# Optimization experiments

Measured on AMD Instinct MI355X. Metric: run time of the kernel, lower is better.

Reference implementation:

```python
import jax, jax.numpy as jnp
import numpy as np

B, S, D = 2, 2048, 2048
H, HD = 16, 128
ROPE_THETA = 10000.0


def _rope_cos_sin(seq_len, head_dim, dtype=jnp.float32):
    inv_freq = 1.0 / (ROPE_THETA ** (jnp.arange(0, head_dim, 2, dtype=jnp.float32) / head_dim))
    t = jnp.arange(seq_len, dtype=jnp.float32)
    freqs = jnp.outer(t, inv_freq)                     # [S, HD/2]
    emb = jnp.concatenate([freqs, freqs], axis=-1)     # [S, HD]
    return jnp.cos(emb).astype(dtype), jnp.sin(emb).astype(dtype)


def _rotate_half(x):
    x1, x2 = jnp.split(x, 2, axis=-1)
    return jnp.concatenate([-x2, x1], axis=-1)


def _apply_rope(x, cos, sin):
    # x: [B, S, H, HD]; cos/sin: [S, HD] -> broadcast over batch and heads
    c = cos[None, :, None, :]
    s = sin[None, :, None, :]
    return x * c + _rotate_half(x) * s


def setup_inputs() -> dict:
    key = jax.random.key(0)
    ks = jax.random.split(key, 6)
    scale = 1.0 / np.sqrt(D)
    hidden_states = jax.random.normal(ks[0], (B, S, D), dtype=jnp.float32)
    # causal additive mask: 0 on/below diagonal, large negative above
    neg = jnp.finfo(jnp.float32).min
    causal = jnp.where(jnp.tril(jnp.ones((S, S), dtype=bool)), 0.0, neg)
    attention_mask = jnp.broadcast_to(causal[None, None, :, :], (B, 1, S, S)).astype(jnp.float32)
    Wq = jax.random.normal(ks[1], (D, D), dtype=jnp.float32) * scale
    Wk = jax.random.normal(ks[2], (D, D), dtype=jnp.float32) * scale
    Wv = jax.random.normal(ks[3], (D, D), dtype=jnp.float32) * scale
    Wo = jax.random.normal(ks[4], (D, D), dtype=jnp.float32) * scale
    return {"hidden_states": hidden_states, "attention_mask": attention_mask,
            "Wq": Wq, "Wk": Wk, "Wv": Wv, "Wo": Wo}


def reference(hidden_states, attention_mask, Wq, Wk, Wv, Wo):
    b, s, d = hidden_states.shape
    # projections (torch Linear: x @ W^T)
    q = (hidden_states @ Wq.T).reshape(b, s, H, HD)
    k = (hidden_states @ Wk.T).reshape(b, s, H, HD)
    v = (hidden_states @ Wv.T).reshape(b, s, H, HD)
    cos, sin = _rope_cos_sin(s, HD, hidden_states.dtype)
    q = _apply_rope(q, cos, sin)
    k = _apply_rope(k, cos, sin)
    # naive attention, [B, H, S, S] scores materialized as in the original
    scores = jnp.einsum('bqhd,bkhd->bhqk', q, k) / np.sqrt(HD)
    scores = scores + attention_mask
    attn = jax.nn.softmax(scores, axis=-1)
    out = jnp.einsum('bhqk,bkhd->bqhd', attn, v).reshape(b, s, d)
    return out @ Wo.T
```

## Files before the change

### kernel.cpp

```cpp
#include <hip/hip_runtime.h>
#include <hip/hip_bf16.h>

typedef __hip_bfloat16 bf16;
typedef __attribute__((ext_vector_type(8))) short s16x8;
typedef __attribute__((ext_vector_type(4))) float f32x4;
typedef __attribute__((ext_vector_type(16))) float f32x16;

#define MFMA16(a, b, c) __builtin_amdgcn_mfma_f32_16x16x32_bf16(a, b, c, 0, 0, 0)
#define MFMA32(a, b, c) __builtin_amdgcn_mfma_f32_32x32x16_bf16(a, b, c, 0, 0, 0)

#define GLL16(gsrc, ldst)                                                                 \
  __builtin_amdgcn_global_load_lds(                                                       \
      (const __attribute__((address_space(1))) unsigned int*)(gsrc),                      \
      (__attribute__((address_space(3))) unsigned int*)(ldst), 16, 0, 0)

#define VMCNT(n) asm volatile("s_waitcnt vmcnt(" #n ")" ::: "memory")
#define BARRIER() __builtin_amdgcn_s_barrier()

static constexpr int S_LEN = 2048;
static constexpr int D_DIM = 2048;
static constexpr int NY = 6144;

union BF4 { ushort4 u; bf16 b[4]; };

__device__ inline unsigned pack2(float a, float b) {
  union { bf16 h[2]; unsigned u; } x;
  x.h[0] = __float2bfloat16(a);
  x.h[1] = __float2bfloat16(b);
  return x.u;
}

__global__ void convert_all(const float* __restrict__ X, const float* __restrict__ Wq,
                            const float* __restrict__ Wk, const float* __restrict__ Wv,
                            const float* __restrict__ Wo, bf16* __restrict__ Xb,
                            bf16* __restrict__ Wb, bf16* __restrict__ Wob,
                            float* __restrict__ cosT, float* __restrict__ sinT) {
  int gid = blockIdx.x * 256 + threadIdx.x;
  if (gid < 6291456) {
    int i4 = gid * 4;
    const float* src;
    bf16* dst;
    int off;
    if (i4 < 8388608) {
      src = X; dst = Xb; off = i4;
    } else {
      int j = i4 - 8388608;
      int seg = j >> 22;
      off = j & 4194303;
      if (seg == 0) { src = Wq; dst = Wb; }
      else if (seg == 1) { src = Wk; dst = Wb + 4194304; }
      else if (seg == 2) { src = Wv; dst = Wb + 8388608; }
      else { src = Wo; dst = Wob; }
    }
    float4 v = *(const float4*)(src + off);
    BF4 o;
    o.b[0] = __float2bfloat16(v.x);
    o.b[1] = __float2bfloat16(v.y);
    o.b[2] = __float2bfloat16(v.z);
    o.b[3] = __float2bfloat16(v.w);
    *(ushort4*)(dst + off) = o.u;
  } else {
    int t4 = (gid - 6291456) * 4;
    if (t4 < 131072) {
#pragma unroll
      for (int k = 0; k < 4; ++k) {
        int i = t4 + k;
        int d = i & 63, s = i >> 6;
        float inv = powf(10000.0f, -(float)d * (1.0f / 64.0f));
        float ang = (float)s * inv;
        cosT[i] = cosf(ang);
        sinT[i] = sinf(ang);
      }
    }
  }
}

__global__ __launch_bounds__(256) void rope_tv(bf16* __restrict__ Y,
                                               const float* __restrict__ cosT,
                                               const float* __restrict__ sinT,
                                               bf16* __restrict__ Vt) {
  __shared__ bf16 tile[32][36];
  const int bid = blockIdx.x;
  const int t = threadIdx.x;
  if (bid < 8192) {
    int idx = bid * 256 + t;
    int quad = idx & 15;
    int h = (idx >> 4) & 15;
    int m = (idx >> 8) & 4095;
    int g = idx >> 20;
    int s = m & (S_LEN - 1);
    int d0 = quad * 4;
    float sc = g ? 1.0f : 0.08838834764831845f;
    bf16* p = Y + (size_t)m * NY + g * D_DIM + h * 128 + d0;
    BF4 lo, hi, olo, ohi;
    lo.u = *(const ushort4*)p;
    hi.u = *(const ushort4*)(p + 64);
    float4 c = *(const float4*)(cosT + s * 64 + d0);
    float4 sn = *(const float4*)(sinT + s * 64 + d0);
    float cc[4] = {c.x, c.y, c.z, c.w};
    float ss[4] = {sn.x, sn.y, sn.z, sn.w};
#pragma unroll
    for (int i = 0; i < 4; ++i) {
      float x1 = __bfloat162float(lo.b[i]);
      float x2 = __bfloat162float(hi.b[i]);
      olo.b[i] = __float2bfloat16((x1 * cc[i] - x2 * ss[i]) * sc);
      ohi.b[i] = __float2bfloat16((x2 * cc[i] + x1 * ss[i]) * sc);
    }
    *(ushort4*)p = olo.u;
    *(ushort4*)(p + 64) = ohi.u;
  } else {
    int id = bid - 8192;
    int bx = id & 63, by = (id >> 6) & 3, bh = id >> 8;
    int b = bh >> 4, h = bh & 15;
    int s0 = bx * 32, d0 = by * 32;
    int r = t >> 3;
    int c4 = (t & 7) * 4;
    BF4 in;
    in.u = *(const ushort4*)(Y + (size_t)(b * S_LEN + s0 + r) * NY + 4096 + h * 128 + d0 + c4);
    *(ushort4*)(&tile[r][c4]) = in.u;
    __syncthreads();
    BF4 o;
#pragma unroll
    for (int i = 0; i < 4; ++i) o.b[i] = tile[c4 + i][r];
    *(ushort4*)(Vt + (size_t)bh * 128 * S_LEN + (size_t)(d0 + r) * S_LEN + s0 + c4) = o.u;
  }
}

__device__ inline void storeC(float* p, float v) { *p = v; }
__device__ inline void storeC(bf16* p, float v) { *p = __float2bfloat16(v); }

template <typename OutT>
__global__ __launch_bounds__(512, 2) void gemm_fine(const bf16* __restrict__ A,
                                                    const bf16* __restrict__ Bm,
                                                    OutT* __restrict__ C, int K, int lda,
                                                    int ldb, int ldc, int mt) {
  __shared__ __align__(16) char lds[147456];
  char* b0 = lds;
  char* b1 = lds + 49152;
  char* b2 = lds + 98304;
  const int tid = threadIdx.x;
  const int lane = tid & 63;
  const int w = tid >> 6;
  const int wm = w >> 2, wn = w & 3;
  const int l15 = lane & 15, lh4 = lane >> 4;
  const int xr = l15 & 7;
  const int xo0 = ((lh4 ^ xr) << 4);
  const int xo1 = (((4 + lh4) ^ xr) << 4);

  const int nwg = gridDim.x;
  const int bid = blockIdx.x;
  const int swz = (bid & 7) * (nwg >> 3) + (bid >> 3);
  const int bm = swz % mt, bn = swz / mt;
  const int row0 = bm * 128, col0 = bn * 256;

  const int srow = w * 8 + (lane >> 3);
  const int scol = ((lane & 7) ^ (lane >> 3)) * 8;
  const bf16* gA = A + (size_t)(row0 + srow) * lda + scol;
  const bf16* gB = Bm + (size_t)(col0 + srow) * ldb + scol;
  const int ldst = w * 1024;

  f32x4 acc[4][4];
#pragma unroll
  for (int i = 0; i < 4; ++i)
#pragma unroll
    for (int j = 0; j < 4; ++j) acc[i][j] = (f32x4){0.f, 0.f, 0.f, 0.f};

  s16x8 af[4], bfr[4];

#define PH_READ(BUF, XO)                                                          \
  _Pragma("unroll") for (int ii = 0; ii < 4; ++ii)                                \
      af[ii] = *(const s16x8*)((BUF) + (wm * 64 + ii * 16 + l15) * 128 + (XO));   \
  _Pragma("unroll") for (int jj = 0; jj < 4; ++jj)                                \
      bfr[jj] = *(const s16x8*)((BUF) + 16384 + (wn * 64 + jj * 16 + l15) * 128 + (XO));
#define PH_FMA()                                                                  \
  __builtin_amdgcn_s_setprio(1);                                                  \
  _Pragma("unroll") for (int jj = 0; jj < 4; ++jj)                                \
  _Pragma("unroll") for (int ii = 0; ii < 4; ++ii)                                \
      acc[ii][jj] = MFMA16(af[ii], bfr[jj], acc[ii][jj]);                         \
  __builtin_amdgcn_s_setprio(0);
#define STAGE_T(BUF, kS)                                                          \
  GLL16(gA + (kS), (BUF) + ldst);                                                 \
  GLL16(gA + (size_t)64 * lda + (kS), (BUF) + 8192 + ldst);                       \
  GLL16(gB + (kS), (BUF) + 16384 + ldst);                                         \
  GLL16(gB + (size_t)64 * ldb + (kS), (BUF) + 24576 + ldst);                      \
  GLL16(gB + (size_t)128 * ldb + (kS), (BUF) + 32768 + ldst);                     \
  GLL16(gB + (size_t)192 * ldb + (kS), (BUF) + 40960 + ldst);
#define TILE_MAIN(RBUF, SBUF, kS)                                                 \
  PH_READ(RBUF, xo0);                                                             \
  GLL16(gA + (kS), (SBUF) + ldst);                                                \
  GLL16(gA + (size_t)64 * lda + (kS), (SBUF) + 8192 + ldst);                      \
  GLL16(gB + (kS), (SBUF) + 16384 + ldst);                                        \
  BARRIER();                                                                      \
  PH_FMA();                                                                       \
  BARRIER();                                                                      \
  PH_READ(RBUF, xo1);                                                             \
  GLL16(gB + (size_t)64 * ldb + (kS), (SBUF) + 24576 + ldst);                     \
  GLL16(gB + (size_t)128 * ldb + (kS), (SBUF) + 32768 + ldst);                    \
  GLL16(gB + (size_t)192 * ldb + (kS), (SBUF) + 40960 + ldst);                    \
  BARRIER();                                                                      \
  PH_FMA();                                                                       \
  VMCNT(6);                                                                       \
  BARRIER();

  STAGE_T(b0, 0);
  STAGE_T(b1, 64);
  VMCNT(6);
  BARRIER();

  const int NT = K >> 6;
  for (int t = 0; t < NT - 2; t += 3) {
    TILE_MAIN(b0, b2, (size_t)(t + 2) * 64);
    TILE_MAIN(b1, b0, (size_t)(t + 3) * 64);
    TILE_MAIN(b2, b1, (size_t)(t + 4) * 64);
  }
  PH_READ(b0, xo0);
  BARRIER();
  PH_FMA();
  BARRIER();
  PH_READ(b0, xo1);
  BARRIER();
  PH_FMA();
  VMCNT(0);
  BARRIER();
  PH_READ(b1, xo0);
  BARRIER();
  PH_FMA();
  BARRIER();
  PH_READ(b1, xo1);
  BARRIER();
  PH_FMA();
#undef PH_READ
#undef PH_FMA
#undef STAGE_T
#undef TILE_MAIN

#pragma unroll
  for (int mi = 0; mi < 4; ++mi)
#pragma unroll
    for (int ni = 0; ni < 4; ++ni) {
      int gr = row0 + wm * 64 + mi * 16 + lh4 * 4;
      int gc = col0 + wn * 64 + ni * 16 + l15;
#pragma unroll
      for (int rr = 0; rr < 4; ++rr)
        storeC(&C[(size_t)(gr + rr) * ldc + gc], acc[mi][ni][rr]);
    }
}

__global__ __launch_bounds__(256, 2) void attn_fwd(const bf16* __restrict__ Y,
                                                   const bf16* __restrict__ Vt,
                                                   bf16* __restrict__ At) {
  __shared__ __align__(16) char smem[65536];

  const int idx = blockIdx.x;
  const int qt = 15 - (idx >> 5);
  const int bh = idx & 31;
  const int b = bh >> 4, h = bh & 15;
  const int tid = threadIdx.x;
  const int lane = tid & 63;
  const int w = tid >> 6;
  const int l31 = lane & 31;
  const int hi = lane >> 5;
  const int q0w = qt * 128 + w * 32;
  const int q = q0w + l31;

  s16x8 qf[8];
  {
    const bf16* qb = Y + (size_t)(b * S_LEN + q) * NY + h * 128 + hi * 8;
#pragma unroll
    for (int s = 0; s < 8; ++s) qf[s] = *(const s16x8*)(qb + s * 16);
  }

  f32x16 O[4];
#pragma unroll
  for (int d = 0; d < 4; ++d)
#pragma unroll
    for (int e = 0; e < 16; ++e) O[d][e] = 0.f;
  float m_run = -3.0e38f, l_run = 0.f;

  const bf16* Kbase = Y + (size_t)(b * S_LEN) * NY + 2048 + h * 128;
  const bf16* Vbase = Vt + (size_t)bh * 128 * S_LEN;
  const int tmax = 2 * qt + 1;

  const int rk_ = w * 4 + (lane >> 4);
  const int ck_ = lane & 15;
  const int dv_ = w * 8 + (lane >> 3);
  const int cv_ = lane & 7;

#define STAGE_KV(T, BASE)                                                         \
  {                                                                               \
    const int kv0s = (T)*64;                                                      \
    _Pragma("unroll") for (int j = 0; j < 4; ++j) {                               \
      int rk = j * 16 + rk_;                                                      \
      GLL16(Kbase + (size_t)(kv0s + rk) * NY + ((ck_ ^ (rk & 15)) * 8),           \
            (BASE) + (j * 4096 + w * 1024));                                      \
      int dv = j * 32 + dv_;                                                      \
      GLL16(Vbase + (size_t)dv * S_LEN + kv0s + ((cv_ ^ (dv & 7)) * 8),           \
            (BASE) + 16384 + (j * 4096 + w * 1024));                              \
    }                                                                             \
  }

  STAGE_KV(0, smem);

  for (int t = 0; t <= tmax; ++t) {
    const int kv0 = t * 64;
    const char* cur = smem + (t & 1) * 32768;
    BARRIER();
    if (t < tmax) {
      STAGE_KV(t + 1, smem + ((t + 1) & 1) * 32768);
      VMCNT(8);
    } else {
      VMCNT(0);
    }
    BARRIER();
    if (kv0 > q0w + 31) continue;

    float sv[32];
#pragma unroll
    for (int tt = 0; tt < 2; ++tt) {
      f32x16 sa;
#pragma unroll
      for (int e = 0; e < 16; ++e) sa[e] = 0.f;
      const int rk = tt * 32 + l31;
      const char* kr = cur + rk * 256;
      const int xr = (rk & 15) << 4;
#pragma unroll
      for (int s = 0; s < 8; ++s) {
        s16x8 kf = *(const s16x8*)(kr + ((s * 32 + hi * 16) ^ xr));
        sa = MFMA32(kf, qf[s], sa);
      }
#pragma unroll
      for (int e = 0; e < 16; ++e) sv[tt * 16 + e] = sa[e];
    }

    if (kv0 + 63 > q0w) {
#pragma unroll
      for (int tt = 0; tt < 2; ++tt)
#pragma unroll
        for (int r = 0; r < 16; ++r) {
          int kvr = kv0 + tt * 32 + (r & 3) + 8 * (r >> 2) + 4 * hi;
          if (kvr > q) sv[tt * 16 + r] = -3.0e38f;
        }
    }

    float mx[16];
#pragma unroll
    for (int i = 0; i < 16; ++i) mx[i] = fmaxf(sv[i], sv[i + 16]);
#pragma unroll
    for (int st = 8; st >= 1; st >>= 1)
#pragma unroll
      for (int i = 0; i < 8; ++i)
        if (i < st) mx[i] = fmaxf(mx[i], mx[i + st]);
    float pmax = fmaxf(mx[0], __shfl_xor(mx[0], 32, 64));

    bool need = pmax > m_run + 8.0f;
    if (__any(need)) {
      float newm = fmaxf(m_run, pmax);
      float ef = __expf(m_run - newm);
      m_run = newm;
      l_run *= ef;
#pragma unroll
      for (int d = 0; d < 4; ++d)
#pragma unroll
        for (int e = 0; e < 16; ++e) O[d][e] *= ef;
    }

    float rsum = 0.f;
#pragma unroll
    for (int i = 0; i < 32; ++i) {
      sv[i] = __expf(sv[i] - m_run);
      rsum += sv[i];
    }
    rsum += __shfl_xor(rsum, 32, 64);
    l_run += rsum;

    unsigned pw[4][4];
#pragma unroll
    for (int tt = 0; tt < 2; ++tt) {
      const int bs = tt * 16;
      unsigned x01 = pack2(sv[bs + 0], sv[bs + 1]);
      unsigned x23 = pack2(sv[bs + 2], sv[bs + 3]);
      unsigned x45 = pack2(sv[bs + 4], sv[bs + 5]);
      unsigned x67 = pack2(sv[bs + 6], sv[bs + 7]);
      unsigned y01 = pack2(sv[bs + 8], sv[bs + 9]);
      unsigned y23 = pack2(sv[bs + 10], sv[bs + 11]);
      unsigned y45 = pack2(sv[bs + 12], sv[bs + 13]);
      unsigned y67 = pack2(sv[bs + 14], sv[bs + 15]);
      unsigned sx01 = __shfl_xor(x01, 32, 64), sx23 = __shfl_xor(x23, 32, 64);
      unsigned sx45 = __shfl_xor(x45, 32, 64), sx67 = __shfl_xor(x67, 32, 64);
      unsigned sy01 = __shfl_xor(y01, 32, 64), sy23 = __shfl_xor(y23, 32, 64);
      unsigned sy45 = __shfl_xor(y45, 32, 64), sy67 = __shfl_xor(y67, 32, 64);
      pw[tt * 2][0] = hi ? sx45 : x01;
      pw[tt * 2][1] = hi ? sx67 : x23;
      pw[tt * 2][2] = hi ? x45 : sx01;
      pw[tt * 2][3] = hi ? x67 : sx23;
      pw[tt * 2 + 1][0] = hi ? sy45 : y01;
      pw[tt * 2 + 1][1] = hi ? sy67 : y23;
      pw[tt * 2 + 1][2] = hi ? y45 : sy01;
      pw[tt * 2 + 1][3] = hi ? y67 : sy23;
    }

#pragma unroll
    for (int dt = 0; dt < 4; ++dt) {
      const int d = dt * 32 + l31;
      const char* vr = cur + 16384 + d * 128;
      const int xv = (d & 7) << 4;
#pragma unroll
      for (int sl = 0; sl < 4; ++sl) {
        s16x8 vf = *(const s16x8*)(vr + ((sl * 32 + hi * 16) ^ xv));
        union { unsigned u[4]; s16x8 v; } pb;
        pb.u[0] = pw[sl][0];
        pb.u[1] = pw[sl][1];
        pb.u[2] = pw[sl][2];
        pb.u[3] = pw[sl][3];
        O[dt] = MFMA32(vf, pb.v, O[dt]);
      }
    }
  }
#undef STAGE_KV

  __syncthreads();
  const float inv = 1.0f / l_run;
  {
    const int orow = w * 32 + l31;
    const int xo = (orow & 15) << 4;
    char* obase = (char*)smem + orow * 256;
#pragma unroll
    for (int dt = 0; dt < 4; ++dt)
#pragma unroll
      for (int r = 0; r < 16; ++r) {
        int d = dt * 32 + (r & 3) + 8 * (r >> 2) + 4 * hi;
        *(bf16*)(obase + ((d * 2) ^ xo)) = __float2bfloat16(O[dt][r] * inv);
      }
  }
  __syncthreads();
  bf16* dst = At + (size_t)(b * S_LEN + qt * 128) * D_DIM + h * 128;
#pragma unroll
  for (int j = 0; j < 8; ++j) {
    int id = j * 256 + tid;
    int rr = id >> 4, cc = id & 15;
    int4 val = *(const int4*)((char*)smem + rr * 256 + ((cc * 16) ^ ((rr & 15) << 4)));
    *(int4*)(dst + (size_t)rr * D_DIM + cc * 8) = val;
  }
}

extern "C" void kernel_launch(void* const* d_in, const int* in_sizes, int n_in,
                              void* d_out, int out_size, void* d_ws, size_t ws_size,
                              hipStream_t stream) {
  const float* X = (const float*)d_in[0];
  const float* Wq = (const float*)d_in[2];
  const float* Wk = (const float*)d_in[3];
  const float* Wv = (const float*)d_in[4];
  const float* Wo = (const float*)d_in[5];
  float* out = (float*)d_out;
  char* ws = (char*)d_ws;

  bf16* Xb = (bf16*)(ws);
  bf16* Wb = (bf16*)(ws + 16777216);
  bf16* Wob = (bf16*)(ws + 41943040);
  bf16* Y = (bf16*)(ws + 50331648);
  bf16* Vt = (bf16*)(ws + 100663296);
  bf16* At = (bf16*)(ws + 117440512);
  float* cosT = (float*)(ws + 134217728);
  float* sinT = (float*)(ws + 134742016);

  convert_all<<<24704, 256, 0, stream>>>(X, Wq, Wk, Wv, Wo, Xb, Wb, Wob, cosT, sinT);

  gemm_fine<bf16><<<768, 512, 0, stream>>>(Xb, Wb, Y, 2048, 2048, 2048, 6144, 32);
  rope_tv<<<16384, 256, 0, stream>>>(Y, cosT, sinT, Vt);
  attn_fwd<<<512, 256, 0, stream>>>(Y, Vt, At);
  gemm_fine<float><<<256, 512, 0, stream>>>(At, Wob, out, 2048, 2048, 2048, 2048, 32);
}
```

Measured before the change: 253.5 us.

## Add 256x256 QK projection GEMM, exp2 softmax, and permlane32 swap

Adds a new 256x256-tile bf16 GEMM with double-buffered LDS staging and quarter-tile MFMA phases, used for the Q and K projections, while the V projection stays on the existing fine GEMM. The log2(e) factor is folded into the Q scale during RoPE so that softmax can use exp2 instead of exp, with the rescale threshold adjusted to match. The lane-swap shuffles that pack P for the PV MFMA are replaced by v_permlane32_swap instructions. These aim to raise GEMM data reuse and trim ALU and shuffle work in attention. The cost is higher register and LDS pressure in the new GEMM and a small precision difference from exp2.

```diff
diff --git a/kernel.cpp b/kernel.cpp
--- a/kernel.cpp
+++ b/kernel.cpp
@@ -90,7 +90,7 @@
     int g = idx >> 20;
     int s = m & (S_LEN - 1);
     int d0 = quad * 4;
-    float sc = g ? 1.0f : 0.08838834764831845f;
+    float sc = g ? 1.0f : 0.08838834764831845f * 1.4426950408889634f;
     bf16* p = Y + (size_t)m * NY + g * D_DIM + h * 128 + d0;
     BF4 lo, hi, olo, ohi;
     lo.u = *(const ushort4*)p;
@@ -128,6 +128,158 @@
 
 __device__ inline void storeC(float* p, float v) { *p = v; }
 __device__ inline void storeC(bf16* p, float v) { *p = __float2bfloat16(v); }
+
+__global__ __launch_bounds__(512, 2) void gemm256(const bf16* __restrict__ A,
+                                                  const bf16* __restrict__ Bm,
+                                                  bf16* __restrict__ C, int K, int lda,
+                                                  int ldb, int ldc, int mt) {
+  __shared__ __align__(16) char lds[131072];
+  char* A0buf = lds;
+  char* B0buf = lds + 32768;
+  char* A1buf = lds + 65536;
+  char* B1buf = lds + 98304;
+  const int tid = threadIdx.x;
+  const int lane = tid & 63;
+  const int w = tid >> 6;
+  const int wm = w >> 2, wn = w & 3;
+  const int l15 = lane & 15, lh4 = lane >> 4;
+  const int xr = l15 & 7;
+  const int xo0 = ((lh4 ^ xr) << 4);
+  const int xo1 = (((4 + lh4) ^ xr) << 4);
+
+  const int nwg = gridDim.x;
+  const int bid = blockIdx.x;
+  const int swz = (bid & 7) * (nwg >> 3) + (bid >> 3);
+  const int bm = swz % mt, bn = swz / mt;
+  const int row0 = bm * 256, col0 = bn * 256;
+
+  const int srow8 = lane >> 3;
+  const int scol = ((lane & 7) ^ srow8) * 8;
+  const bf16* gA_s = A + (size_t)(row0 + w * 8 + srow8) * lda + scol;
+  const bf16* gB_s = Bm + (size_t)(col0 + (w >> 2) * 64 + (w & 3) * 8 + srow8) * ldb + scol;
+  const int ldst = w * 1024;
+
+#define STAGE_A(bufa, rh, k0)                                                     \
+  {                                                                               \
+    GLL16(gA_s + (size_t)((rh)*64) * lda + (k0), (bufa) + (rh)*16384 + ldst);     \
+    GLL16(gA_s + (size_t)((rh)*64 + 128) * lda + (k0),                            \
+          (bufa) + (rh)*16384 + 8192 + ldst);                                     \
+  }
+#define STAGE_B(bufb, ch, k0)                                                     \
+  {                                                                               \
+    GLL16(gB_s + (size_t)((ch)*32) * ldb + (k0), (bufb) + (ch)*16384 + ldst);     \
+    GLL16(gB_s + (size_t)((ch)*32 + 128) * ldb + (k0),                            \
+          (bufb) + (ch)*16384 + 8192 + ldst);                                     \
+  }
+
+  f32x4 acc[8][4];
+#pragma unroll
+  for (int i = 0; i < 8; ++i)
+#pragma unroll
+    for (int j = 0; j < 4; ++j) acc[i][j] = (f32x4){0.f, 0.f, 0.f, 0.f};
+
+  s16x8 af[4][2];
+  s16x8 bfr[2][2];
+
+#define READ_AH(bufa, rh)                                                         \
+  _Pragma("unroll") for (int ii = 0; ii < 4; ++ii) {                              \
+    const char* p_ = (bufa) + (rh)*16384 + (wm * 64 + ii * 16 + l15) * 128;       \
+    af[ii][0] = *(const s16x8*)(p_ + xo0);                                        \
+    af[ii][1] = *(const s16x8*)(p_ + xo1);                                        \
+  }
+#define READ_BH(bufb, ch)                                                         \
+  _Pragma("unroll") for (int jj = 0; jj < 2; ++jj) {                              \
+    const char* p_ = (bufb) + (ch)*16384 + (wn * 32 + jj * 16 + l15) * 128;       \
+    bfr[jj][0] = *(const s16x8*)(p_ + xo0);                                       \
+    bfr[jj][1] = *(const s16x8*)(p_ + xo1);                                       \
+  }
+#define QUAD(rh, ch)                                                              \
+  __builtin_amdgcn_s_setprio(1);                                                  \
+  _Pragma("unroll") for (int jj = 0; jj < 2; ++jj)                                \
+  _Pragma("unroll") for (int ii = 0; ii < 4; ++ii)                                \
+  _Pragma("unroll") for (int ks = 0; ks < 2; ++ks)                                \
+      acc[(rh)*4 + ii][(ch)*2 + jj] =                                             \
+          MFMA16(af[ii][ks], bfr[jj][ks], acc[(rh)*4 + ii][(ch)*2 + jj]);         \
+  __builtin_amdgcn_s_setprio(0);
+
+  STAGE_A(A0buf, 0, 0);
+  STAGE_B(B0buf, 0, 0);
+  STAGE_B(B0buf, 1, 0);
+  STAGE_A(A0buf, 1, 0);
+  STAGE_A(A1buf, 0, 64);
+  STAGE_B(B1buf, 1, 64);
+  STAGE_A(A1buf, 1, 64);
+  VMCNT(6);
+  BARRIER();
+
+  const int NI = K >> 7;
+  for (int i = 0; i < NI; ++i) {
+    const int kT1 = (2 * i + 1) << 6;
+    const int kT2 = (2 * i + 2) << 6;
+    const int kT3 = (2 * i + 3) << 6;
+    const bool nl = (i + 1 < NI);
+    READ_AH(A0buf, 0);
+    READ_BH(B0buf, 0);
+    STAGE_B(B1buf, 0, kT1);
+    BARRIER();
+    QUAD(0, 0);
+    BARRIER();
+    READ_BH(B0buf, 1);
+    if (nl) STAGE_A(A0buf, 0, kT2);
+    BARRIER();
+    QUAD(0, 1);
+    BARRIER();
+    READ_AH(A0buf, 1);
+    if (nl) STAGE_B(B0buf, 1, kT2);
+    BARRIER();
+    QUAD(1, 1);
+    BARRIER();
+    READ_BH(B0buf, 0);
+    if (nl) STAGE_A(A0buf, 1, kT2);
+    BARRIER();
+    QUAD(1, 0);
+    if (nl) { VMCNT(6); } else { VMCNT(0); }
+    BARRIER();
+    READ_AH(A1buf, 0);
+    READ_BH(B1buf, 0);
+    if (nl) STAGE_B(B0buf, 0, kT2);
+    BARRIER();
+    QUAD(0, 0);
+    BARRIER();
+    READ_BH(B1buf, 1);
+    if (nl) STAGE_A(A1buf, 0, kT3);
+    BARRIER();
+    QUAD(0, 1);
+    BARRIER();
+    READ_AH(A1buf, 1);
+    if (nl) STAGE_B(B1buf, 1, kT3);
+    BARRIER();
+    QUAD(1, 1);
+    BARRIER();
+    READ_BH(B1buf, 0);
+    if (nl) STAGE_A(A1buf, 1, kT3);
+    BARRIER();
+    QUAD(1, 0);
+    if (nl) { VMCNT(6); }
+    BARRIER();
+  }
+#undef STAGE_A
+#undef STAGE_B
+#undef READ_AH
+#undef READ_BH
+#undef QUAD
+
+#pragma unroll
+  for (int ri = 0; ri < 8; ++ri)
+#pragma unroll
+    for (int cj = 0; cj < 4; ++cj) {
+      int gr = row0 + wm * 128 + ri * 16 + lh4 * 4;
+      int gc = col0 + wn * 64 + cj * 16 + l15;
+#pragma unroll
+      for (int rr = 0; rr < 4; ++rr)
+        C[(size_t)(gr + rr) * ldc + gc] = __float2bfloat16(acc[ri][cj][rr]);
+    }
+}
 
 template <typename OutT>
 __global__ __launch_bounds__(512, 2) void gemm_fine(const bf16* __restrict__ A,
@@ -352,10 +504,10 @@
         if (i < st) mx[i] = fmaxf(mx[i], mx[i + st]);
     float pmax = fmaxf(mx[0], __shfl_xor(mx[0], 32, 64));
 
-    bool need = pmax > m_run + 8.0f;
+    bool need = pmax > m_run + 11.54f;
     if (__any(need)) {
       float newm = fmaxf(m_run, pmax);
-      float ef = __expf(m_run - newm);
+      float ef = exp2f(m_run - newm);
       m_run = newm;
       l_run *= ef;
 #pragma unroll
@@ -367,7 +519,7 @@
     float rsum = 0.f;
 #pragma unroll
     for (int i = 0; i < 32; ++i) {
-      sv[i] = __expf(sv[i] - m_run);
+      sv[i] = exp2f(sv[i] - m_run);
       rsum += sv[i];
     }
     rsum += __shfl_xor(rsum, 32, 64);
@@ -385,18 +537,18 @@
       unsigned y23 = pack2(sv[bs + 10], sv[bs + 11]);
       unsigned y45 = pack2(sv[bs + 12], sv[bs + 13]);
       unsigned y67 = pack2(sv[bs + 14], sv[bs + 15]);
-      unsigned sx01 = __shfl_xor(x01, 32, 64), sx23 = __shfl_xor(x23, 32, 64);
-      unsigned sx45 = __shfl_xor(x45, 32, 64), sx67 = __shfl_xor(x67, 32, 64);
-      unsigned sy01 = __shfl_xor(y01, 32, 64), sy23 = __shfl_xor(y23, 32, 64);
-      unsigned sy45 = __shfl_xor(y45, 32, 64), sy67 = __shfl_xor(y67, 32, 64);
-      pw[tt * 2][0] = hi ? sx45 : x01;
-      pw[tt * 2][1] = hi ? sx67 : x23;
-      pw[tt * 2][2] = hi ? x45 : sx01;
-      pw[tt * 2][3] = hi ? x67 : sx23;
-      pw[tt * 2 + 1][0] = hi ? sy45 : y01;
-      pw[tt * 2 + 1][1] = hi ? sy67 : y23;
-      pw[tt * 2 + 1][2] = hi ? y45 : sy01;
-      pw[tt * 2 + 1][3] = hi ? y67 : sy23;
+      asm volatile("v_permlane32_swap_b32 %0, %1" : "+v"(x01), "+v"(x45));
+      asm volatile("v_permlane32_swap_b32 %0, %1" : "+v"(x23), "+v"(x67));
+      asm volatile("v_permlane32_swap_b32 %0, %1" : "+v"(y01), "+v"(y45));
+      asm volatile("v_permlane32_swap_b32 %0, %1" : "+v"(y23), "+v"(y67));
+      pw[tt * 2][0] = x01;
+      pw[tt * 2][1] = x23;
+      pw[tt * 2][2] = x45;
+      pw[tt * 2][3] = x67;
+      pw[tt * 2 + 1][0] = y01;
+      pw[tt * 2 + 1][1] = y23;
+      pw[tt * 2 + 1][2] = y45;
+      pw[tt * 2 + 1][3] = y67;
     }
 
 #pragma unroll
@@ -465,7 +617,9 @@
 
   convert_all<<<24704, 256, 0, stream>>>(X, Wq, Wk, Wv, Wo, Xb, Wb, Wob, cosT, sinT);
 
-  gemm_fine<bf16><<<768, 512, 0, stream>>>(Xb, Wb, Y, 2048, 2048, 2048, 6144, 32);
+  gemm256<<<256, 512, 0, stream>>>(Xb, Wb, Y, 2048, 2048, 2048, 6144, 16);
+  gemm_fine<bf16><<<256, 512, 0, stream>>>(Xb, Wb + (size_t)4096 * 2048, Y + 4096,
+                                           2048, 2048, 2048, 6144, 32);
   rope_tv<<<16384, 256, 0, stream>>>(Y, cosT, sinT, Vt);
   attn_fwd<<<512, 256, 0, stream>>>(Y, Vt, At);
   gemm_fine<float><<<256, 512, 0, stream>>>(At, Wob, out, 2048, 2048, 2048, 2048, 32);
```

Result: faster. 247.8 us (-2.3%).
